# Performance work log

Hardware: AMD Instinct MI355X
Metric: run time of the kernel (lower is better)

The kernel has to match this reference:

```python
import jax, jax.numpy as jnp
import numpy as np

B, T, S, D, H, DK = 2, 2048, 2048, 1024, 16, 64


def setup_inputs() -> dict:
    key = jax.random.key(0)
    ks = jax.random.split(key, 11)
    s = 1.0 / np.sqrt(D)
    return {
        "query": jax.random.normal(ks[0], (B, T, D), jnp.float32),
        "value": jax.random.normal(ks[1], (B, S, D), jnp.float32),
        "key": jax.random.normal(ks[2], (B, S, D), jnp.float32),
        "Wq": jax.random.normal(ks[3], (D, H, DK), jnp.float32) * s,
        "bq": jnp.zeros((H, DK), jnp.float32),
        "Wk": jax.random.normal(ks[4], (D, H, DK), jnp.float32) * s,
        "bk": jnp.zeros((H, DK), jnp.float32),
        "Wv": jax.random.normal(ks[5], (D, H, DK), jnp.float32) * s,
        "bv": jnp.zeros((H, DK), jnp.float32),
        "Wo": jax.random.normal(ks[6], (H, DK, D), jnp.float32) * (1.0 / np.sqrt(H * DK)),
        "bo": jnp.zeros((D,), jnp.float32),
    }


def reference(query, value, key, Wq, bq, Wk, bk, Wv, bv, Wo, bo):
    # Projections: (B, seq, D) x (D, H, DK) -> (B, seq, H, DK)
    q = jnp.einsum("btd,dhk->bthk", query, Wq) + bq
    k = jnp.einsum("bsd,dhk->bshk", key, Wk) + bk
    v = jnp.einsum("bsd,dhk->bshk", value, Wv) + bv
    # Scaled dot-product attention (keras scales query by 1/sqrt(key_dim))
    q = q * (1.0 / np.sqrt(DK)).astype(np.float32)
    scores = jnp.einsum("bshk,bthk->bhts", k, q)  # (B, H, T, S)
    probs = jax.nn.softmax(scores, axis=-1)
    attn = jnp.einsum("bhts,bshk->bthk", probs, v)  # (B, T, H, DK)
    # Output projection back to model dim
    out = jnp.einsum("bthk,hkd->btd", attn, Wo) + bo
    return out
```

## Files before the change

kernel.cpp:

```cpp
#include <hip/hip_runtime.h>
#include <math.h>

#define BB  2
#define TT  2048
#define SSQ 2048
#define DD  1024
#define HH  16
#define DKK 64
#define MM  (BB*TT)
#define NN  (HH*DKK)

typedef __attribute__((ext_vector_type(8))) short short8;
typedef __attribute__((ext_vector_type(4))) float f32x4;

__device__ __forceinline__ short f2bf(float x) {
    unsigned u = __builtin_bit_cast(unsigned, x);
    unsigned r = (u + 0x7FFFu + ((u >> 16) & 1u)) >> 16;
    return (short)r;
}

__device__ __forceinline__ void glds16(const void* g, void* l) {
    __builtin_amdgcn_global_load_lds(
        (const __attribute__((address_space(1))) void*)g,
        (__attribute__((address_space(3))) void*)l, 16, 0, 0);
}

__global__ __launch_bounds__(256)
void to_bf16_acts(const float* __restrict__ a0, const float* __restrict__ a1,
                  const float* __restrict__ a2,
                  short* __restrict__ o0, short* __restrict__ o1,
                  short* __restrict__ o2)
{
    int z = blockIdx.y;
    const float* in = (z == 0) ? a0 : (z == 1) ? a1 : a2;
    short* out = (z == 0) ? o0 : (z == 1) ? o1 : o2;
    size_t i0 = ((size_t)blockIdx.x * 256 + threadIdx.x) * 8;
    f32x4 f0 = *(const f32x4*)(in + i0);
    f32x4 f1 = *(const f32x4*)(in + i0 + 4);
    short8 v;
#pragma unroll
    for (int j = 0; j < 4; j++) v[j] = f2bf(f0[j]);
#pragma unroll
    for (int j = 0; j < 4; j++) v[4 + j] = f2bf(f1[j]);
    *(short8*)(out + i0) = v;
}

__global__ __launch_bounds__(256)
void wtrans(const float* __restrict__ w0, const float* __restrict__ w1,
            const float* __restrict__ w2, const float* __restrict__ w3,
            short* __restrict__ t0, short* __restrict__ t1,
            short* __restrict__ t2, short* __restrict__ t3)
{
    __shared__ float Ls[64][65];
    int z = blockIdx.z;
    const float* in = (z == 0) ? w0 : (z == 1) ? w1 : (z == 2) ? w2 : w3;
    short* out = (z == 0) ? t0 : (z == 1) ? t1 : (z == 2) ? t2 : t3;
    const int r0 = blockIdx.y * 64, c0 = blockIdx.x * 64;
    const int t = threadIdx.x;
    const int r = t >> 2, c4 = t & 3;

    const float* src = in + (size_t)(r0 + r) * DD + c0 + c4 * 16;
#pragma unroll
    for (int i = 0; i < 4; i++) {
        f32x4 f = *(const f32x4*)(src + i * 4);
#pragma unroll
        for (int j = 0; j < 4; j++) Ls[r][c4 * 16 + i * 4 + j] = f[j];
    }
    __syncthreads();

    short8 va, vb;
#pragma unroll
    for (int j = 0; j < 8; j++) va[j] = f2bf(Ls[c4 * 16 + j][r]);
#pragma unroll
    for (int j = 0; j < 8; j++) vb[j] = f2bf(Ls[c4 * 16 + 8 + j][r]);
    short* dst = out + (size_t)(c0 + r) * DD + r0 + c4 * 16;
    *(short8*)dst = va;
    *(short8*)(dst + 8) = vb;
}

__global__ __launch_bounds__(256)
void vtrans(const short* __restrict__ in, short* __restrict__ out)
{
    __shared__ short Ls[64][72];
    const int bh = blockIdx.y;
    const int t0 = blockIdx.x * 64;
    const int tid = threadIdx.x;
    const int r = tid >> 2, c4 = tid & 3;

    const short* src = in + ((size_t)bh * TT + t0 + r) * DKK + c4 * 16;
    *(short8*)&Ls[r][c4 * 16]     = *(const short8*)(src);
    *(short8*)&Ls[r][c4 * 16 + 8] = *(const short8*)(src + 8);
    __syncthreads();

    short8 a, b;
#pragma unroll
    for (int j = 0; j < 8; j++) a[j] = Ls[c4 * 16 + j][r];
#pragma unroll
    for (int j = 0; j < 8; j++) b[j] = Ls[c4 * 16 + 8 + j][r];
    short* dst = out + ((size_t)bh * DKK + r) * SSQ + t0 + c4 * 16;
    *(short8*)dst = a;
    *(short8*)(dst + 8) = b;
}

__device__ __forceinline__ void gemm_core(const short* __restrict__ A,
                                          const short* __restrict__ Bt,
                                          int m0, int n0,
                                          short* As, short* Bs,
                                          f32x4 (&acc)[4][4])
{
    const int tid = threadIdx.x;
    const int w = tid >> 6, l = tid & 63;
    const int l15 = l & 15, quad = l >> 4;
    const int wm = w >> 1, wn = w & 1;

#pragma unroll
    for (int i = 0; i < 4; i++)
#pragma unroll
        for (int j = 0; j < 4; j++) acc[i][j] = (f32x4){0.f, 0.f, 0.f, 0.f};

    const int r = tid >> 2, cseg = tid & 3;
    const short* gA = A + (size_t)(m0 + r) * DD + cseg * 8;
    const short* gB = Bt + (size_t)(n0 + r) * DD + cseg * 8;
    short* ldsA = As + w * 512;
    short* ldsB = Bs + w * 512;

    for (int k0 = 0; k0 < DD; k0 += 32) {
        glds16(gA + k0,                 ldsA);
        glds16(gA + (size_t)64 * DD + k0, ldsA + 2048);
        glds16(gB + k0,                 ldsB);
        glds16(gB + (size_t)64 * DD + k0, ldsB + 2048);
        __syncthreads();

        short8 bF[4];
#pragma unroll
        for (int ni = 0; ni < 4; ni++)
            bF[ni] = *(const short8*)&Bs[(wn * 64 + ni * 16 + l15) * 32 + quad * 8];
#pragma unroll
        for (int mi = 0; mi < 4; mi++) {
            short8 aF = *(const short8*)&As[(wm * 64 + mi * 16 + l15) * 32 + quad * 8];
#pragma unroll
            for (int ni = 0; ni < 4; ni++)
                acc[mi][ni] = __builtin_amdgcn_mfma_f32_16x16x32_bf16(aF, bF[ni], acc[mi][ni], 0, 0, 0);
        }
        __syncthreads();
    }
}

__global__ __launch_bounds__(256, 3)
void gemm_qkv(const short* __restrict__ Aq, const short* __restrict__ Ak,
              const short* __restrict__ Av,
              const short* __restrict__ Wqt, const short* __restrict__ Wkt,
              const short* __restrict__ Wvt,
              const float* __restrict__ bq, const float* __restrict__ bk,
              const float* __restrict__ bv,
              short* __restrict__ Qb, short* __restrict__ Kb,
              short* __restrict__ Vtmp)
{
    __shared__ short As[128 * 32];
    __shared__ short Bs[128 * 32];
    const int z = blockIdx.z;
    const short* A  = (z == 0) ? Aq : (z == 1) ? Ak : Av;
    const short* Bt = (z == 0) ? Wqt : (z == 1) ? Wkt : Wvt;
    const float* bias = (z == 0) ? bq : (z == 1) ? bk : bv;
    short* dst = (z == 0) ? Qb : (z == 1) ? Kb : Vtmp;
    const int m0 = blockIdx.y * 128, n0 = blockIdx.x * 128;

    f32x4 acc[4][4];
    gemm_core(A, Bt, m0, n0, As, Bs, acc);

    const int tid = threadIdx.x;
    const int w = tid >> 6, l = tid & 63;
    const int l15 = l & 15, quad = l >> 4;
    const int wm = w >> 1, wn = w & 1;
    const float scale = (z == 0) ? 0.1803368801f : 1.0f;

#pragma unroll
    for (int mi = 0; mi < 4; mi++) {
#pragma unroll
        for (int reg = 0; reg < 4; reg++) {
            int m = m0 + wm * 64 + mi * 16 + quad * 4 + reg;
            int b = m >> 11, t = m & 2047;
#pragma unroll
            for (int ni = 0; ni < 4; ni++) {
                int n = n0 + wn * 64 + ni * 16 + l15;
                float vv = (acc[mi][ni][reg] + bias[n]) * scale;
                int h = n >> 6, dk = n & 63;
                dst[((size_t)(b * HH + h) * TT + t) * DKK + dk] = f2bf(vv);
            }
        }
    }
}

__global__ __launch_bounds__(256, 3)
void gemm_out(const short* __restrict__ Ab, const short* __restrict__ Wot,
              const float* __restrict__ bo, float* __restrict__ out)
{
    __shared__ short As[128 * 32];
    __shared__ short Bs[128 * 32];
    const int m0 = blockIdx.y * 128, n0 = blockIdx.x * 128;

    f32x4 acc[4][4];
    gemm_core(Ab, Wot, m0, n0, As, Bs, acc);

    const int tid = threadIdx.x;
    const int w = tid >> 6, l = tid & 63;
    const int l15 = l & 15, quad = l >> 4;
    const int wm = w >> 1, wn = w & 1;

#pragma unroll
    for (int mi = 0; mi < 4; mi++) {
#pragma unroll
        for (int reg = 0; reg < 4; reg++) {
            int m = m0 + wm * 64 + mi * 16 + quad * 4 + reg;
#pragma unroll
            for (int ni = 0; ni < 4; ni++) {
                int n = n0 + wn * 64 + ni * 16 + l15;
                out[(size_t)m * DD + n] = acc[mi][ni][reg] + bo[n];
            }
        }
    }
}

__global__ __launch_bounds__(256, 2)
void attn_mfma(const short* __restrict__ Qb, const short* __restrict__ Kb,
               const short* __restrict__ Vbt, short* __restrict__ Ab)
{
    __shared__ short QPs[128 * 72];
    __shared__ short Ks[64 * 72];
    __shared__ short Vs[64 * 72];

    const int tid = threadIdx.x;
    const int w = tid >> 6, l = tid & 63;
    const int l15 = l & 15, quad = l >> 4;
    const int bh = blockIdx.y;
    const int t0 = blockIdx.x * 128;
    const size_t hb = (size_t)bh * SSQ * DKK;
    const int r = tid >> 2, c4 = tid & 3;

    {
        int r2 = tid >> 1, half = tid & 1;
        const short* g = Qb + hb + (size_t)(t0 + r2) * 64 + half * 32;
        short* s = QPs + r2 * 72 + half * 32;
        *(short8*)(s + 0)  = *(const short8*)(g + 0);
        *(short8*)(s + 8)  = *(const short8*)(g + 8);
        *(short8*)(s + 16) = *(const short8*)(g + 16);
        *(short8*)(s + 24) = *(const short8*)(g + 24);
    }
    __threadfence_block();
    short8 qf[2][2];
#pragma unroll
    for (int mf = 0; mf < 2; mf++)
#pragma unroll
        for (int kk = 0; kk < 2; kk++)
            qf[mf][kk] = *(const short8*)&QPs[(32 * w + 16 * mf + l15) * 72 + kk * 32 + quad * 8];

    const short* gkb = Kb + hb + (size_t)r * 64 + c4 * 16;
    const short* gvb = Vbt + hb + (size_t)r * SSQ + c4 * 16;
    short8 kr0 = *(const short8*)(gkb + 0);
    short8 kr1 = *(const short8*)(gkb + 8);
    short8 vr0 = *(const short8*)(gvb + 0);
    short8 vr1 = *(const short8*)(gvb + 8);

    f32x4 o[2][4];
#pragma unroll
    for (int mf = 0; mf < 2; mf++)
#pragma unroll
        for (int j = 0; j < 4; j++) o[mf][j] = (f32x4){0.f, 0.f, 0.f, 0.f};
    float lsum[2][4];
#pragma unroll
    for (int mf = 0; mf < 2; mf++)
#pragma unroll
        for (int j = 0; j < 4; j++) lsum[mf][j] = 0.f;

    short* sk = Ks + r * 72 + c4 * 16;
    short* sv = Vs + r * 72 + c4 * 16;

    for (int s0 = 0; s0 < SSQ; s0 += 64) {
        __syncthreads();
        *(short8*)(sk + 0) = kr0;
        *(short8*)(sk + 8) = kr1;
        *(short8*)(sv + 0) = vr0;
        *(short8*)(sv + 8) = vr1;
        if (s0 + 64 < SSQ) {
            const short* gk = gkb + (size_t)(s0 + 64) * 64;
            const short* gv = gvb + (s0 + 64);
            kr0 = *(const short8*)(gk + 0);
            kr1 = *(const short8*)(gk + 8);
            vr0 = *(const short8*)(gv + 0);
            vr1 = *(const short8*)(gv + 8);
        }
        __syncthreads();

        f32x4 sc[2][4];
#pragma unroll
        for (int mf = 0; mf < 2; mf++)
#pragma unroll
            for (int j = 0; j < 4; j++) sc[mf][j] = (f32x4){0.f, 0.f, 0.f, 0.f};
#pragma unroll
        for (int kk = 0; kk < 2; kk++) {
#pragma unroll
            for (int np = 0; np < 4; np++) {
                short8 bK = *(const short8*)&Ks[(16 * np + l15) * 72 + kk * 32 + quad * 8];
                sc[0][np] = __builtin_amdgcn_mfma_f32_16x16x32_bf16(qf[0][kk], bK, sc[0][np], 0, 0, 0);
                sc[1][np] = __builtin_amdgcn_mfma_f32_16x16x32_bf16(qf[1][kk], bK, sc[1][np], 0, 0, 0);
            }
        }

#pragma unroll
        for (int mf = 0; mf < 2; mf++) {
            int prow = (32 * w + 16 * mf + quad * 4) * 72 + l15;
#pragma unroll
            for (int reg = 0; reg < 4; reg++) {
                int pr = prow + reg * 72;
#pragma unroll
                for (int np = 0; np < 4; np++) {
                    float p = __builtin_amdgcn_exp2f(sc[mf][np][reg]);
                    QPs[pr + 16 * np] = (short)(__builtin_bit_cast(unsigned, p) >> 16);
                    lsum[mf][reg] += p;
                }
            }
        }
        __threadfence_block();

#pragma unroll
        for (int kk = 0; kk < 2; kk++) {
            short8 aP0 = *(const short8*)&QPs[(32 * w + l15) * 72 + kk * 32 + quad * 8];
            short8 aP1 = *(const short8*)&QPs[(32 * w + 16 + l15) * 72 + kk * 32 + quad * 8];
#pragma unroll
            for (int np = 0; np < 4; np++) {
                short8 bV = *(const short8*)&Vs[(16 * np + l15) * 72 + kk * 32 + quad * 8];
                o[0][np] = __builtin_amdgcn_mfma_f32_16x16x32_bf16(aP0, bV, o[0][np], 0, 0, 0);
                o[1][np] = __builtin_amdgcn_mfma_f32_16x16x32_bf16(aP1, bV, o[1][np], 0, 0, 0);
            }
        }
    }

    const int b = bh >> 4, h = bh & 15;
#pragma unroll
    for (int mf = 0; mf < 2; mf++) {
#pragma unroll
        for (int reg = 0; reg < 4; reg++) {
            float ls = lsum[mf][reg];
            ls += __shfl_xor(ls, 1);
            ls += __shfl_xor(ls, 2);
            ls += __shfl_xor(ls, 4);
            ls += __shfl_xor(ls, 8);
            float inv = 1.f / ls;
            int t = t0 + 32 * w + 16 * mf + quad * 4 + reg;
#pragma unroll
            for (int np = 0; np < 4; np++) {
                Ab[((size_t)(b * TT + t) * HH + h) * DKK + 16 * np + l15] =
                    f2bf(o[mf][np][reg] * inv);
            }
        }
    }
}

extern "C" void kernel_launch(void* const* d_in, const int* in_sizes, int n_in,
                              void* d_out, int out_size, void* d_ws, size_t ws_size,
                              hipStream_t stream)
{
    const float* query = (const float*)d_in[0];
    const float* value = (const float*)d_in[1];
    const float* key   = (const float*)d_in[2];
    const float* Wq    = (const float*)d_in[3];
    const float* bq    = (const float*)d_in[4];
    const float* Wk    = (const float*)d_in[5];
    const float* bk    = (const float*)d_in[6];
    const float* Wv    = (const float*)d_in[7];
    const float* bv    = (const float*)d_in[8];
    const float* Wo    = (const float*)d_in[9];
    const float* bo    = (const float*)d_in[10];
    float* out = (float*)d_out;

    const size_t actE = (size_t)MM * DD;
    const size_t wE   = (size_t)DD * NN;
    short* p = (short*)d_ws;
    short* Aq   = p; p += actE;
    short* Ak   = p; p += actE;
    short* Av   = p; p += actE;
    short* Wqt  = p; p += wE;
    short* Wkt  = p; p += wE;
    short* Wvt  = p; p += wE;
    short* Wot  = p; p += wE;
    short* Qb   = p; p += actE;
    short* Kb   = p; p += actE;
    short* Vtmp = p; p += actE;
    short* Vbt  = p; p += actE;
    short* Ab   = p; p += actE;

    dim3 blk(256);

    to_bf16_acts<<<dim3((unsigned)(actE / 2048), 3), blk, 0, stream>>>(
        query, key, value, Aq, Ak, Av);

    wtrans<<<dim3(16, 16, 4), blk, 0, stream>>>(Wq, Wk, Wv, Wo, Wqt, Wkt, Wvt, Wot);

    gemm_qkv<<<dim3(NN / 128, MM / 128, 3), blk, 0, stream>>>(
        Aq, Ak, Av, Wqt, Wkt, Wvt, bq, bk, bv, Qb, Kb, Vtmp);

    vtrans<<<dim3(TT / 64, BB * HH), blk, 0, stream>>>(Vtmp, Vbt);

    attn_mfma<<<dim3(TT / 128, BB * HH), blk, 0, stream>>>(Qb, Kb, Vbt, Ab);

    gemm_out<<<dim3(DD / 128, MM / 128), blk, 0, stream>>>(Ab, Wot, bo, out);
}
```

Before: 241.0 us.

## Double-buffer K/V tiles, transpose score MFMA for packed P stores, add setprio

The attention kernel now double-buffers the K and V shared-memory tiles, which removes one __syncthreads per iteration. It also swaps the MFMA operands so the score tile comes out transposed. Each lane can then pack four bf16 probabilities into a single 8-byte LDS store, and the row sums collapse to one per fragment, reduced across quads at the end. s_setprio is raised around the MFMA blocks. Together these aim to cut barrier stalls and LDS store instructions, at the cost of more shared memory, which may affect occupancy.

Measured after the change: 233.4 us. 1.03x faster.

```diff
diff --git a/kernel.cpp b/kernel.cpp
--- a/kernel.cpp
+++ b/kernel.cpp
@@ -12,6 +12,7 @@
 
 typedef __attribute__((ext_vector_type(8))) short short8;
 typedef __attribute__((ext_vector_type(4))) float f32x4;
+typedef __attribute__((ext_vector_type(2))) unsigned int u32x2;
 
 __device__ __forceinline__ short f2bf(float x) {
     unsigned u = __builtin_bit_cast(unsigned, x);
@@ -226,8 +227,8 @@
                const short* __restrict__ Vbt, short* __restrict__ Ab)
 {
     __shared__ short QPs[128 * 72];
-    __shared__ short Ks[64 * 72];
-    __shared__ short Vs[64 * 72];
+    __shared__ short Ks[2][64 * 72];
+    __shared__ short Vs[2][64 * 72];
 
     const int tid = threadIdx.x;
     const int w = tid >> 6, l = tid & 63;
@@ -266,21 +267,17 @@
     for (int mf = 0; mf < 2; mf++)
 #pragma unroll
         for (int j = 0; j < 4; j++) o[mf][j] = (f32x4){0.f, 0.f, 0.f, 0.f};
-    float lsum[2][4];
-#pragma unroll
-    for (int mf = 0; mf < 2; mf++)
-#pragma unroll
-        for (int j = 0; j < 4; j++) lsum[mf][j] = 0.f;
-
-    short* sk = Ks + r * 72 + c4 * 16;
-    short* sv = Vs + r * 72 + c4 * 16;
+    float lsum[2] = {0.f, 0.f};
+
+    short* skb = &Ks[0][0] + r * 72 + c4 * 16;
+    short* svb = &Vs[0][0] + r * 72 + c4 * 16;
 
     for (int s0 = 0; s0 < SSQ; s0 += 64) {
-        __syncthreads();
-        *(short8*)(sk + 0) = kr0;
-        *(short8*)(sk + 8) = kr1;
-        *(short8*)(sv + 0) = vr0;
-        *(short8*)(sv + 8) = vr1;
+        const int bo = (s0 & 64) ? (64 * 72) : 0;
+        *(short8*)(skb + bo)     = kr0;
+        *(short8*)(skb + bo + 8) = kr1;
+        *(short8*)(svb + bo)     = vr0;
+        *(short8*)(svb + bo + 8) = vr1;
         if (s0 + 64 < SSQ) {
             const short* gk = gkb + (size_t)(s0 + 64) * 64;
             const short* gv = gvb + (s0 + 64);
@@ -291,66 +288,80 @@
         }
         __syncthreads();
 
-        f32x4 sc[2][4];
-#pragma unroll
-        for (int mf = 0; mf < 2; mf++)
-#pragma unroll
-            for (int j = 0; j < 4; j++) sc[mf][j] = (f32x4){0.f, 0.f, 0.f, 0.f};
+        const short* kb_ = &Ks[0][0] + bo;
+        const short* vb_ = &Vs[0][0] + bo;
+
+        f32x4 sc[4][2];
+#pragma unroll
+        for (int np = 0; np < 4; np++)
+#pragma unroll
+            for (int mf = 0; mf < 2; mf++) sc[np][mf] = (f32x4){0.f, 0.f, 0.f, 0.f};
+        __builtin_amdgcn_s_setprio(1);
 #pragma unroll
         for (int kk = 0; kk < 2; kk++) {
 #pragma unroll
             for (int np = 0; np < 4; np++) {
-                short8 bK = *(const short8*)&Ks[(16 * np + l15) * 72 + kk * 32 + quad * 8];
-                sc[0][np] = __builtin_amdgcn_mfma_f32_16x16x32_bf16(qf[0][kk], bK, sc[0][np], 0, 0, 0);
-                sc[1][np] = __builtin_amdgcn_mfma_f32_16x16x32_bf16(qf[1][kk], bK, sc[1][np], 0, 0, 0);
-            }
-        }
+                short8 aK = *(const short8*)&kb_[(16 * np + l15) * 72 + kk * 32 + quad * 8];
+                sc[np][0] = __builtin_amdgcn_mfma_f32_16x16x32_bf16(aK, qf[0][kk], sc[np][0], 0, 0, 0);
+                sc[np][1] = __builtin_amdgcn_mfma_f32_16x16x32_bf16(aK, qf[1][kk], sc[np][1], 0, 0, 0);
+            }
+        }
+        __builtin_amdgcn_s_setprio(0);
 
 #pragma unroll
         for (int mf = 0; mf < 2; mf++) {
-            int prow = (32 * w + 16 * mf + quad * 4) * 72 + l15;
-#pragma unroll
-            for (int reg = 0; reg < 4; reg++) {
-                int pr = prow + reg * 72;
-#pragma unroll
-                for (int np = 0; np < 4; np++) {
-                    float p = __builtin_amdgcn_exp2f(sc[mf][np][reg]);
-                    QPs[pr + 16 * np] = (short)(__builtin_bit_cast(unsigned, p) >> 16);
-                    lsum[mf][reg] += p;
-                }
-            }
+            short* pr = QPs + (32 * w + 16 * mf + l15) * 72 + 4 * quad;
+            float ls = lsum[mf];
+#pragma unroll
+            for (int np = 0; np < 4; np++) {
+                float p0 = __builtin_amdgcn_exp2f(sc[np][mf][0]);
+                float p1 = __builtin_amdgcn_exp2f(sc[np][mf][1]);
+                float p2 = __builtin_amdgcn_exp2f(sc[np][mf][2]);
+                float p3 = __builtin_amdgcn_exp2f(sc[np][mf][3]);
+                ls += (p0 + p1) + (p2 + p3);
+                unsigned lo = (__builtin_bit_cast(unsigned, p1) & 0xFFFF0000u) |
+                              (__builtin_bit_cast(unsigned, p0) >> 16);
+                unsigned hi = (__builtin_bit_cast(unsigned, p3) & 0xFFFF0000u) |
+                              (__builtin_bit_cast(unsigned, p2) >> 16);
+                u32x2 uv;
+                uv[0] = lo;
+                uv[1] = hi;
+                *(u32x2*)(pr + 16 * np) = uv;
+            }
+            lsum[mf] = ls;
         }
         __threadfence_block();
 
+        __builtin_amdgcn_s_setprio(1);
 #pragma unroll
         for (int kk = 0; kk < 2; kk++) {
             short8 aP0 = *(const short8*)&QPs[(32 * w + l15) * 72 + kk * 32 + quad * 8];
             short8 aP1 = *(const short8*)&QPs[(32 * w + 16 + l15) * 72 + kk * 32 + quad * 8];
 #pragma unroll
             for (int np = 0; np < 4; np++) {
-                short8 bV = *(const short8*)&Vs[(16 * np + l15) * 72 + kk * 32 + quad * 8];
+                short8 bV = *(const short8*)&vb_[(16 * np + l15) * 72 + kk * 32 + quad * 8];
                 o[0][np] = __builtin_amdgcn_mfma_f32_16x16x32_bf16(aP0, bV, o[0][np], 0, 0, 0);
                 o[1][np] = __builtin_amdgcn_mfma_f32_16x16x32_bf16(aP1, bV, o[1][np], 0, 0, 0);
             }
         }
+        __builtin_amdgcn_s_setprio(0);
     }
 
     const int b = bh >> 4, h = bh & 15;
 #pragma unroll
     for (int mf = 0; mf < 2; mf++) {
+        float ls = lsum[mf];
+        ls += __shfl_xor(ls, 16);
+        ls += __shfl_xor(ls, 32);
+        float inv = 1.f / ls;
 #pragma unroll
         for (int reg = 0; reg < 4; reg++) {
-            float ls = lsum[mf][reg];
-            ls += __shfl_xor(ls, 1);
-            ls += __shfl_xor(ls, 2);
-            ls += __shfl_xor(ls, 4);
-            ls += __shfl_xor(ls, 8);
-            float inv = 1.f / ls;
+            float invr = __shfl(inv, quad * 4 + reg);
             int t = t0 + 32 * w + 16 * mf + quad * 4 + reg;
 #pragma unroll
             for (int np = 0; np < 4; np++) {
                 Ab[((size_t)(b * TT + t) * HH + h) * DKK + 16 * np + l15] =
-                    f2bf(o[mf][np][reg] * inv);
+                    f2bf(o[mf][np][reg] * invr);
             }
         }
     }
```
